# Kernel tuning notes

Hardware: AMD Instinct MI355X
Metric: run time of the kernel (lower is better)

Reference implementation:

```python
import jax, jax.numpy as jnp
import numpy as np

N = 50000
E = 800000
D = 128
EPS = 1e-5


def setup_inputs() -> dict:
    key = jax.random.key(0)
    ks = jax.random.split(key, 12)
    s1 = 1.0 / np.sqrt(2 * D)
    s2 = 1.0 / np.sqrt(D)
    return {
        "x": jax.random.normal(ks[0], (N, D), dtype=jnp.float32),
        "edge_index": jax.random.randint(ks[1], (2, E), 0, N, dtype=jnp.int32),
        # message MLP: Linear(2D->D), SiLU, Linear(D->D)
        "wm1": jax.random.uniform(ks[2], (2 * D, D), jnp.float32, -s1, s1),
        "bm1": jax.random.uniform(ks[3], (D,), jnp.float32, -s1, s1),
        "wm2": jax.random.uniform(ks[4], (D, D), jnp.float32, -s2, s2),
        "bm2": jax.random.uniform(ks[5], (D,), jnp.float32, -s2, s2),
        # update MLP: Linear(2D->D), SiLU, Linear(D->D)
        "wu1": jax.random.uniform(ks[6], (2 * D, D), jnp.float32, -s1, s1),
        "bu1": jax.random.uniform(ks[7], (D,), jnp.float32, -s1, s1),
        "wu2": jax.random.uniform(ks[8], (D, D), jnp.float32, -s2, s2),
        "bu2": jax.random.uniform(ks[9], (D,), jnp.float32, -s2, s2),
        # LayerNorm affine
        "gamma": jnp.ones((D,), jnp.float32),
        "beta": jnp.zeros((D,), jnp.float32),
    }


def reference(x, edge_index, wm1, bm1, wm2, bm2, wu1, bu1, wu2, bu2, gamma, beta):
    row, col = edge_index[0], edge_index[1]
    # gather endpoints and build message input [E, 2D]
    msg_in = jnp.concatenate([x[row], x[col]], axis=-1)
    h = jax.nn.silu(msg_in @ wm1 + bm1)
    messages = h @ wm2 + bm2  # [E, D]
    # scatter-add aggregate into destination rows
    aggr = jax.ops.segment_sum(messages, row, num_segments=x.shape[0])  # [N, D]
    upd_in = jnp.concatenate([x, aggr], axis=-1)  # [N, 2D]
    u = jax.nn.silu(upd_in @ wu1 + bu1)
    out = u @ wu2 + bu2  # [N, D]
    # residual + LayerNorm
    y = x + out
    mu = jnp.mean(y, axis=-1, keepdims=True)
    var = jnp.var(y, axis=-1, keepdims=True)
    yn = (y - mu) * jax.lax.rsqrt(var + EPS)
    return yn * gamma + beta
```

## Files before the change

### kernel.cpp

```cpp
#include <hip/hip_runtime.h>
#include <hip/hip_bf16.h>

#define NN 50000
#define EE 800000
#define DD 128
#define TILES (EE / 64)
#define NB_SCAN ((NN + 255) / 256)

typedef __attribute__((ext_vector_type(8))) short bf8v;
typedef __attribute__((ext_vector_type(4))) float f4v;
typedef __attribute__((ext_vector_type(4))) unsigned int u4v;

static __device__ __forceinline__ unsigned int bpack2(float lo, float hi) {
    union { __hip_bfloat162 h2; unsigned int u; } c;
    c.h2 = __float22bfloat162_rn(float2{lo, hi});
    return c.u;
}
static __device__ __forceinline__ u4v pack8(f4v a, f4v b) {
    u4v r;
    r[0] = bpack2(a[0], a[1]); r[1] = bpack2(a[2], a[3]);
    r[2] = bpack2(b[0], b[1]); r[3] = bpack2(b[2], b[3]);
    return r;
}
static __device__ __forceinline__ short f2bf_s(float f) {
    union { __hip_bfloat16 h; short s; } c;
    c.h = __float2bfloat16(f);
    return c.s;
}
static __device__ __forceinline__ float bf_lo(unsigned int u) {
    union { unsigned int u; float f; } c; c.u = u << 16; return c.f;
}
static __device__ __forceinline__ float bf_hi(unsigned int u) {
    union { unsigned int u; float f; } c; c.u = u & 0xffff0000u; return c.f;
}
static __device__ __forceinline__ float silu(float v) {
    return v * __builtin_amdgcn_rcpf(1.f + __expf(-v));
}

__global__ __launch_bounds__(256) void setup_kernel(
    const float* __restrict__ wm1, const float* __restrict__ wm2,
    const float* __restrict__ wu1, const float* __restrict__ wu2,
    short* __restrict__ out, int* __restrict__ cnt, float* __restrict__ aggr) {
    int idx = blockIdx.x * 256 + threadIdx.x;
    {
        const float* src; int l;
        if      (idx < 32768) { src = wm1; l = idx; }
        else if (idx < 49152) { src = wm2; l = idx - 32768; }
        else if (idx < 81920) { src = wu1; l = idx - 49152; }
        else                  { src = wu2; l = idx - 81920; }
        int e    = l & 7;
        int lane = (l >> 3) & 63;
        int ntg  = (l >> 9) & 7;
        int kc   = l >> 12;
        out[idx] = f2bf_s(src[(kc * 32 + (lane >> 4) * 8 + e) * DD + ntg * 16 + (lane & 15)]);
    }
    for (int i = idx; i < NN; i += 98304) cnt[i] = 0;
    f4v z = (f4v){0.f, 0.f, 0.f, 0.f};
    for (int i = idx; i < NN * DD / 4; i += 98304) ((f4v*)aggr)[i] = z;
}

__global__ __launch_bounds__(256) void hist_rank_kernel(const int* __restrict__ ei,
                                                        int* __restrict__ cnt,
                                                        int* __restrict__ rank) {
    int e = blockIdx.x * 256 + threadIdx.x;
    if (e < EE) rank[e] = atomicAdd(&cnt[ei[e]], 1);
}

__global__ __launch_bounds__(256) void scanA_kernel(const int* __restrict__ cnt,
                                                    int* __restrict__ bsum) {
    __shared__ int sd[256];
    int t = threadIdx.x;
    int i = blockIdx.x * 256 + t;
    sd[t] = (i < NN) ? cnt[i] : 0;
    __syncthreads();
    for (int off = 128; off > 0; off >>= 1) {
        if (t < off) sd[t] += sd[t + off];
        __syncthreads();
    }
    if (t == 0) bsum[blockIdx.x] = sd[0];
}

__global__ __launch_bounds__(256) void scanB_kernel(const int* __restrict__ bsum,
                                                    int* __restrict__ bscan) {
    __shared__ int sd[256];
    int t = threadIdx.x;
    int v = (t < NB_SCAN) ? bsum[t] : 0;
    sd[t] = v;
    __syncthreads();
    for (int off = 1; off < 256; off <<= 1) {
        int u = (t >= off) ? sd[t - off] : 0;
        __syncthreads();
        sd[t] += u;
        __syncthreads();
    }
    if (t < NB_SCAN) bscan[t] = sd[t] - v;
}

__global__ __launch_bounds__(256) void scanC_kernel(const int* __restrict__ cnt,
                                                    const int* __restrict__ bscan,
                                                    int* __restrict__ cursor,
                                                    int* __restrict__ rows) {
    __shared__ int sd[256];
    int t = threadIdx.x;
    int i = blockIdx.x * 256 + t;
    int v = (i < NN) ? cnt[i] : 0;
    sd[t] = v;
    __syncthreads();
    for (int off = 1; off < 256; off <<= 1) {
        int u = (t >= off) ? sd[t - off] : 0;
        __syncthreads();
        sd[t] += u;
        __syncthreads();
    }
    if (i < NN) {
        int c0 = bscan[blockIdx.x] + sd[t] - v;
        cursor[i] = c0;
        for (int k = 0; k < v; ++k) rows[c0 + k] = i;
    }
}

__global__ __launch_bounds__(256) void scatter_col_rank_kernel(const int* __restrict__ ei,
                                                               const int* __restrict__ cursor,
                                                               const int* __restrict__ rank,
                                                               int* __restrict__ srtc) {
    int e = blockIdx.x * 256 + threadIdx.x;
    if (e < EE) srtc[cursor[ei[e]] + rank[e]] = ei[EE + e];
}

__global__ __launch_bounds__(256) void scatter_col_atomic_kernel(const int* __restrict__ ei,
                                                                 int* __restrict__ cursor,
                                                                 int* __restrict__ srtc) {
    int e = blockIdx.x * 256 + threadIdx.x;
    if (e < EE) {
        int pos = atomicAdd(&cursor[ei[e]], 1);
        srtc[pos] = ei[EE + e];
    }
}

__global__ __launch_bounds__(256) void pq_kernel(
    const float* __restrict__ x,
    const short* __restrict__ W1f, const float* __restrict__ bm1,
    short* __restrict__ P, short* __restrict__ Q)
{
    __shared__ char smem[32768];
    const int tid = threadIdx.x;
    const int w = tid >> 6, lane = tid & 63;
    const int rbase = blockIdx.x * 64;
    const int rloc = tid >> 2, s = tid & 3;

    {
        int rg = rbase + rloc;
        int rgc = rg < NN ? rg : NN - 1;
        const float* xr = x + (size_t)rgc * DD + s * 32;
        int swz = (rloc & 7) << 4;
        #pragma unroll
        for (int j = 0; j < 4; ++j) {
            f4v a0 = *(const f4v*)(xr + j * 8);
            f4v a1 = *(const f4v*)(xr + j * 8 + 4);
            *(u4v*)(smem + ((rloc * 256 + s * 64 + j * 16) ^ swz)) = pack8(a0, a1);
        }
    }

    bf8v w1t[4][2], w1b[4][2];
    #pragma unroll
    for (int kc = 0; kc < 4; ++kc)
        #pragma unroll
        for (int nt = 0; nt < 2; ++nt) {
            w1t[kc][nt] = *(const bf8v*)(W1f + (((kc * 8) + (w * 2 + nt)) * 64 + lane) * 8);
            w1b[kc][nt] = *(const bf8v*)(W1f + ((((kc + 4) * 8) + (w * 2 + nt)) * 64 + lane) * 8);
        }
    __syncthreads();

    f4v accP[4][2], accQ[4][2];
    #pragma unroll
    for (int mt = 0; mt < 4; ++mt)
        #pragma unroll
        for (int nt = 0; nt < 2; ++nt) {
            accP[mt][nt] = (f4v){0.f, 0.f, 0.f, 0.f};
            accQ[mt][nt] = (f4v){0.f, 0.f, 0.f, 0.f};
        }
    #pragma unroll
    for (int kc = 0; kc < 4; ++kc) {
        bf8v a[4];
        int kb = kc * 64 + (lane >> 4) * 16;
        #pragma unroll
        for (int mt = 0; mt < 4; ++mt) {
            int row = mt * 16 + (lane & 15);
            a[mt] = *(const bf8v*)(smem + ((row * 256 + kb) ^ ((row & 7) << 4)));
        }
        #pragma unroll
        for (int mt = 0; mt < 4; ++mt)
            #pragma unroll
            for (int nt = 0; nt < 2; ++nt) {
                accP[mt][nt] = __builtin_amdgcn_mfma_f32_16x16x32_bf16(a[mt], w1t[kc][nt], accP[mt][nt], 0, 0, 0);
                accQ[mt][nt] = __builtin_amdgcn_mfma_f32_16x16x32_bf16(a[mt], w1b[kc][nt], accQ[mt][nt], 0, 0, 0);
            }
    }
    __syncthreads();

    int col0 = w * 32 + (lane & 15);
    float b1a = bm1[col0], b1b = bm1[col0 + 16];
    #pragma unroll
    for (int mt = 0; mt < 4; ++mt)
        #pragma unroll
        for (int nt = 0; nt < 2; ++nt) {
            float bb = nt ? b1b : b1a;
            int col = col0 + nt * 16;
            #pragma unroll
            for (int r = 0; r < 4; ++r) {
                int row = mt * 16 + (lane >> 4) * 4 + r;
                int off = (row * 256 + col * 2) ^ ((row & 7) << 4);
                *(short*)(smem + off)         = f2bf_s(accP[mt][nt][r] + bb);
                *(short*)(smem + 16384 + off) = f2bf_s(accQ[mt][nt][r]);
            }
        }
    __syncthreads();

    {
        int rg = rbase + rloc;
        if (rg < NN) {
            int swz = (rloc & 7) << 4;
            #pragma unroll
            for (int j = 0; j < 4; ++j) {
                int off = (rloc * 256 + s * 64 + j * 16) ^ swz;
                *(u4v*)(P + (size_t)rg * DD + s * 32 + j * 8) = *(const u4v*)(smem + off);
                *(u4v*)(Q + (size_t)rg * DD + s * 32 + j * 8) = *(const u4v*)(smem + 16384 + off);
            }
        }
    }
}

__global__ __launch_bounds__(256, 8) void edge_kernel(
    const short* __restrict__ P, const short* __restrict__ Q,
    const int* __restrict__ rows, const int* __restrict__ srtc,
    const int* __restrict__ ei, int use_sorted,
    const short* __restrict__ W2f, const float* __restrict__ bm2,
    float* __restrict__ aggr)
{
    __shared__ char smem[16384 + 256];
    char* Hs = smem;
    int* rows_s = (int*)(smem + 16384);

    const int tid = threadIdx.x;
    const int w = tid >> 6, lane = tid & 63;
    const int rloc = tid >> 2, s = tid & 3;

    {
        int eg = blockIdx.x * 64 + rloc;
        int r, c;
        if (use_sorted) { r = rows[eg]; c = srtc[eg]; }
        else            { r = ei[eg];   c = ei[EE + eg]; }
        if (s == 0) rows_s[rloc] = r;
        const u4v* pr = (const u4v*)(P + (size_t)r * DD + s * 32);
        const u4v* qr = (const u4v*)(Q + (size_t)c * DD + s * 32);
        int swz = (rloc & 7) << 4;
        #pragma unroll
        for (int j = 0; j < 4; ++j) {
            u4v pj = pr[j], qj = qr[j];
            u4v hv;
            #pragma unroll
            for (int k2 = 0; k2 < 4; ++k2) {
                float lo = silu(bf_lo(pj[k2]) + bf_lo(qj[k2]));
                float hi = silu(bf_hi(pj[k2]) + bf_hi(qj[k2]));
                hv[k2] = bpack2(lo, hi);
            }
            *(u4v*)(Hs + ((rloc * 256 + s * 64 + j * 16) ^ swz)) = hv;
        }
    }

    bf8v w2f[4][2];
    #pragma unroll
    for (int kc = 0; kc < 4; ++kc)
        #pragma unroll
        for (int nt = 0; nt < 2; ++nt)
            w2f[kc][nt] = *(const bf8v*)(W2f + (((kc * 8) + (w * 2 + nt)) * 64 + lane) * 8);
    int col0 = w * 32 + (lane & 15);
    float b2a = bm2[col0], b2b = bm2[col0 + 16];

    __syncthreads();

    f4v acc2[4][2];
    #pragma unroll
    for (int mt = 0; mt < 4; ++mt)
        #pragma unroll
        for (int nt = 0; nt < 2; ++nt)
            acc2[mt][nt] = (f4v){0.f, 0.f, 0.f, 0.f};
    #pragma unroll
    for (int kc = 0; kc < 4; ++kc) {
        bf8v a[4];
        int kb = kc * 64 + (lane >> 4) * 16;
        #pragma unroll
        for (int mt = 0; mt < 4; ++mt) {
            int row = mt * 16 + (lane & 15);
            a[mt] = *(const bf8v*)(Hs + ((row * 256 + kb) ^ ((row & 7) << 4)));
        }
        #pragma unroll
        for (int mt = 0; mt < 4; ++mt)
            #pragma unroll
            for (int nt = 0; nt < 2; ++nt)
                acc2[mt][nt] = __builtin_amdgcn_mfma_f32_16x16x32_bf16(a[mt], w2f[kc][nt], acc2[mt][nt], 0, 0, 0);
    }
    __syncthreads();

    #pragma unroll
    for (int mt = 0; mt < 4; ++mt)
        #pragma unroll
        for (int nt = 0; nt < 2; ++nt) {
            int col = col0 + nt * 16;
            float bb = nt ? b2b : b2a;
            #pragma unroll
            for (int r = 0; r < 4; ++r) {
                int row = mt * 16 + (lane >> 4) * 4 + r;
                *(short*)(Hs + ((row * 256 + col * 2) ^ ((row & 7) << 4))) = f2bf_s(acc2[mt][nt][r] + bb);
            }
        }
    __syncthreads();

    {
        int col = tid & 127;
        int r0 = (tid >> 7) * 32;
        int cur = rows_s[r0];
        float run = 0.f;
        for (int k = 0; k < 32; ++k) {
            int row = r0 + k;
            int d = rows_s[row];
            unsigned short sv = *(const unsigned short*)(Hs + ((row * 256 + col * 2) ^ ((row & 7) << 4)));
            union { unsigned int u; float f; } c; c.u = ((unsigned int)sv) << 16;
            if (d != cur) {
                unsafeAtomicAdd(aggr + (size_t)cur * DD + col, run);
                run = 0.f; cur = d;
            }
            run += c.f;
        }
        unsafeAtomicAdd(aggr + (size_t)cur * DD + col, run);
    }
}

__global__ __launch_bounds__(256, 4) void node_kernel(
    const float* __restrict__ x, const float* __restrict__ aggr,
    const short* __restrict__ U1f, const short* __restrict__ U2f,
    const float* __restrict__ bu1, const float* __restrict__ bu2,
    const float* __restrict__ gmm, const float* __restrict__ bta,
    float* __restrict__ out)
{
    __shared__ char smem[64 * 512 + 2048];
    char* As = smem;
    float* ps  = (float*)(smem + 64 * 512);
    float* ps2 = ps + 256;

    const int tid = threadIdx.x;
    const int w = tid >> 6, lane = tid & 63;
    const int rbase = blockIdx.x * 64;
    const int rloc = tid >> 2, s = tid & 3;

    {
        int rg = rbase + rloc;
        int rgc = rg < NN ? rg : 0;
        const float* xr = x + (size_t)rgc * DD + s * 32;
        const float* ar = aggr + (size_t)rgc * DD + s * 32;
        int swz = (rloc & 7) << 4;
        #pragma unroll
        for (int i2 = 0; i2 < 4; ++i2) {
            f4v a0 = *(const f4v*)(xr + i2 * 8);
            f4v a1 = *(const f4v*)(xr + i2 * 8 + 4);
            int addr = rloc * 512 + s * 64 + i2 * 16;
            *(u4v*)(As + (addr ^ swz)) = pack8(a0, a1);
            f4v b0 = *(const f4v*)(ar + i2 * 8);
            f4v b1 = *(const f4v*)(ar + i2 * 8 + 4);
            int addr2 = rloc * 512 + 256 + s * 64 + i2 * 16;
            *(u4v*)(As + (addr2 ^ swz)) = pack8(b0, b1);
        }
    }

    bf8v u1f[8][2], u2f[4][2];
    #pragma unroll
    for (int kc = 0; kc < 8; ++kc)
        #pragma unroll
        for (int nt = 0; nt < 2; ++nt)
            u1f[kc][nt] = *(const bf8v*)(U1f + (((kc * 8) + (w * 2 + nt)) * 64 + lane) * 8);
    #pragma unroll
    for (int kc = 0; kc < 4; ++kc)
        #pragma unroll
        for (int nt = 0; nt < 2; ++nt)
            u2f[kc][nt] = *(const bf8v*)(U2f + (((kc * 8) + (w * 2 + nt)) * 64 + lane) * 8);

    __syncthreads();

    f4v acc[4][2];
    #pragma unroll
    for (int mt = 0; mt < 4; ++mt)
        #pragma unroll
        for (int nt = 0; nt < 2; ++nt)
            acc[mt][nt] = (f4v){0.f, 0.f, 0.f, 0.f};
    #pragma unroll
    for (int kc = 0; kc < 8; ++kc) {
        bf8v a[4];
        int kb = kc * 64 + (lane >> 4) * 16;
        #pragma unroll
        for (int mt = 0; mt < 4; ++mt) {
            int row = mt * 16 + (lane & 15);
            a[mt] = *(const bf8v*)(As + ((row * 512 + kb) ^ ((row & 7) << 4)));
        }
        #pragma unroll
        for (int mt = 0; mt < 4; ++mt)
            #pragma unroll
            for (int nt = 0; nt < 2; ++nt)
                acc[mt][nt] = __builtin_amdgcn_mfma_f32_16x16x32_bf16(a[mt], u1f[kc][nt], acc[mt][nt], 0, 0, 0);
    }
    __syncthreads();

    int col0 = w * 32 + (lane & 15);
    float b1a = bu1[col0], b1b = bu1[col0 + 16];
    #pragma unroll
    for (int mt = 0; mt < 4; ++mt)
        #pragma unroll
        for (int nt = 0; nt < 2; ++nt) {
            float bb = nt ? b1b : b1a;
            int col = col0 + nt * 16;
            #pragma unroll
            for (int r = 0; r < 4; ++r) {
                float v = silu(acc[mt][nt][r] + bb);
                int row = mt * 16 + (lane >> 4) * 4 + r;
                *(short*)(As + ((row * 256 + col * 2) ^ ((row & 7) << 4))) = f2bf_s(v);
            }
        }
    __syncthreads();

    f4v acc2[4][2];
    #pragma unroll
    for (int mt = 0; mt < 4; ++mt)
        #pragma unroll
        for (int nt = 0; nt < 2; ++nt)
            acc2[mt][nt] = (f4v){0.f, 0.f, 0.f, 0.f};
    #pragma unroll
    for (int kc = 0; kc < 4; ++kc) {
        bf8v a[4];
        int kb = kc * 64 + (lane >> 4) * 16;
        #pragma unroll
        for (int mt = 0; mt < 4; ++mt) {
            int row = mt * 16 + (lane & 15);
            a[mt] = *(const bf8v*)(As + ((row * 256 + kb) ^ ((row & 7) << 4)));
        }
        #pragma unroll
        for (int mt = 0; mt < 4; ++mt)
            #pragma unroll
            for (int nt = 0; nt < 2; ++nt)
                acc2[mt][nt] = __builtin_amdgcn_mfma_f32_16x16x32_bf16(a[mt], u2f[kc][nt], acc2[mt][nt], 0, 0, 0);
    }
    __syncthreads();

    float b2a = bu2[col0], b2b = bu2[col0 + 16];
    #pragma unroll
    for (int mt = 0; mt < 4; ++mt)
        #pragma unroll
        for (int nt = 0; nt < 2; ++nt) {
            int col = col0 + nt * 16;
            float bb = nt ? b2b : b2a;
            #pragma unroll
            for (int r = 0; r < 4; ++r) {
                int rowl = mt * 16 + (lane >> 4) * 4 + r;
                int rg = rbase + rowl;
                int rgc = rg < NN ? rg : 0;
                float xv = x[(size_t)rgc * DD + col];
                float y = acc2[mt][nt][r] + bb + xv;
                *(float*)(As + ((rowl * 512 + col * 4) ^ ((rowl & 7) << 4))) = y;
            }
        }
    __syncthreads();

    {
        int q = tid & 3;
        float s1 = 0.f, s2 = 0.f;
        #pragma unroll
        for (int i = 0; i < 8; ++i) {
            f4v v = *(const f4v*)(As + ((rloc * 512 + q * 128 + i * 16) ^ ((rloc & 7) << 4)));
            s1 += v[0] + v[1] + v[2] + v[3];
            s2 += v[0] * v[0] + v[1] * v[1] + v[2] * v[2] + v[3] * v[3];
        }
        ps[rloc * 4 + q] = s1;
        ps2[rloc * 4 + q] = s2;
    }
    __syncthreads();
    {
        int q = tid & 3;
        float fs  = ps[rloc * 4] + ps[rloc * 4 + 1] + ps[rloc * 4 + 2] + ps[rloc * 4 + 3];
        float fs2 = ps2[rloc * 4] + ps2[rloc * 4 + 1] + ps2[rloc * 4 + 2] + ps2[rloc * 4 + 3];
        float mu  = fs * (1.f / 128.f);
        float var = fs2 * (1.f / 128.f) - mu * mu;
        float inv = rsqrtf(var + 1e-5f);
        int rg = rbase + rloc;
        if (rg < NN) {
            #pragma unroll
            for (int i = 0; i < 8; ++i) {
                int col = q * 32 + i * 4;
                f4v v  = *(const f4v*)(As + ((rloc * 512 + col * 4) ^ ((rloc & 7) << 4)));
                f4v gg = *(const f4v*)(gmm + col);
                f4v bb = *(const f4v*)(bta + col);
                f4v o;
                #pragma unroll
                for (int j = 0; j < 4; ++j)
                    o[j] = (v[j] - mu) * inv * gg[j] + bb[j];
                *(f4v*)(out + (size_t)rg * DD + col) = o;
            }
        }
    }
}

extern "C" void kernel_launch(void* const* d_in, const int* in_sizes, int n_in,
                              void* d_out, int out_size, void* d_ws, size_t ws_size,
                              hipStream_t stream) {
    const float* x    = (const float*)d_in[0];
    const int*   ei   = (const int*)d_in[1];
    const float* wm1  = (const float*)d_in[2];
    const float* bm1  = (const float*)d_in[3];
    const float* wm2  = (const float*)d_in[4];
    const float* bm2  = (const float*)d_in[5];
    const float* wu1  = (const float*)d_in[6];
    const float* bu1  = (const float*)d_in[7];
    const float* wu2  = (const float*)d_in[8];
    const float* bu2  = (const float*)d_in[9];
    const float* gmm  = (const float*)d_in[10];
    const float* bta  = (const float*)d_in[11];
    float* out = (float*)d_out;

    const size_t off_P     = 0;
    const size_t off_Q     = 12800000;
    const size_t off_frags = 25600000;
    const size_t off_cnt   = 25796608;
    const size_t off_cur   = 25996608;
    const size_t off_bsum  = 26196608;
    const size_t off_bscan = 26197632;
    const size_t off_rows  = 26198656;
    const size_t off_srtc  = 29398656;
    const size_t off_rank  = 32598656;
    const size_t need_rank   = 35798656;
    const size_t need_atomic = 32598656;

    char* wsB = (char*)d_ws;
    short* P    = (short*)(wsB + off_P);
    short* Q    = (short*)(wsB + off_Q);
    short* Wf   = (short*)(wsB + off_frags);
    short* W1f  = Wf;
    short* W2f  = Wf + 32768;
    short* U1f  = Wf + 49152;
    short* U2f  = Wf + 81920;
    int*   cnt    = (int*)(wsB + off_cnt);
    int*   cursor = (int*)(wsB + off_cur);
    int*   bsum   = (int*)(wsB + off_bsum);
    int*   bscan  = (int*)(wsB + off_bscan);
    int*   rows   = (int*)(wsB + off_rows);
    int*   srtc   = (int*)(wsB + off_srtc);
    int*   rank   = (int*)(wsB + off_rank);

    float* aggr = (float*)d_out;

    int tier = (ws_size >= need_rank) ? 2 : (ws_size >= need_atomic ? 1 : 0);

    setup_kernel<<<384, 256, 0, stream>>>(wm1, wm2, wu1, wu2, Wf, cnt, aggr);

    int use_sorted = 0;
    if (tier > 0) {
        hist_rank_kernel<<<(EE + 255) / 256, 256, 0, stream>>>(ei, cnt,
            tier == 2 ? rank : srtc );
        scanA_kernel<<<NB_SCAN, 256, 0, stream>>>(cnt, bsum);
        scanB_kernel<<<1, 256, 0, stream>>>(bsum, bscan);
        scanC_kernel<<<NB_SCAN, 256, 0, stream>>>(cnt, bscan, cursor, rows);
        if (tier == 2)
            scatter_col_rank_kernel<<<(EE + 255) / 256, 256, 0, stream>>>(ei, cursor, rank, srtc);
        else
            scatter_col_atomic_kernel<<<(EE + 255) / 256, 256, 0, stream>>>(ei, cursor, srtc);
        use_sorted = 1;
    }

    pq_kernel<<<(NN + 63) / 64, 256, 0, stream>>>(x, W1f, bm1, P, Q);

    edge_kernel<<<TILES, 256, 0, stream>>>(P, Q, rows, srtc, ei, use_sorted, W2f, bm2, aggr);
    node_kernel<<<(NN + 63) / 64, 256, 0, stream>>>(x, aggr, U1f, U2f, bu1, bu2, gmm, bta, out);
}
```

Measured before the change: 196.6 us.

## Merge preprocessing launches into fused kernels and shrink index arrays to 16-bit

Several kernels are merged so fewer launches run. The histogram/rank pass now shares a launch with weight fragment packing and aggr zeroing, and the column scatter shares a launch with the P/Q projection. The block-sum scan is folded into the second scan kernel, and cnt is cleared with a memset. Sorted row and column indices are stored as 16-bit values, halving index traffic in the edge kernel. The tier-1 atomic fallback is dropped. The u16 indices only hold because NN (50000) is below 65536.

```diff
diff --git a/kernel.cpp b/kernel.cpp
--- a/kernel.cpp
+++ b/kernel.cpp
@@ -6,6 +6,9 @@
 #define DD 128
 #define TILES (EE / 64)
 #define NB_SCAN ((NN + 255) / 256)
+#define HIST_BLKS ((EE + 255) / 256)
+#define FRAG_BLKS 384
+#define PQ_BLKS ((NN + 63) / 64)
 
 typedef __attribute__((ext_vector_type(8))) short bf8v;
 typedef __attribute__((ext_vector_type(4))) float f4v;
@@ -37,11 +40,21 @@
     return v * __builtin_amdgcn_rcpf(1.f + __expf(-v));
 }
 
-__global__ __launch_bounds__(256) void setup_kernel(
+__global__ __launch_bounds__(256) void mega1_kernel(
+    const int* __restrict__ ei, int* __restrict__ cnt, int* __restrict__ rank, int do_sort,
     const float* __restrict__ wm1, const float* __restrict__ wm2,
     const float* __restrict__ wu1, const float* __restrict__ wu2,
-    short* __restrict__ out, int* __restrict__ cnt, float* __restrict__ aggr) {
-    int idx = blockIdx.x * 256 + threadIdx.x;
+    short* __restrict__ wf, float* __restrict__ aggr)
+{
+    int b = blockIdx.x;
+    if (b < HIST_BLKS) {
+        if (do_sort) {
+            int e = b * 256 + threadIdx.x;
+            if (e < EE) rank[e] = atomicAdd(&cnt[ei[e]], 1);
+        }
+        return;
+    }
+    int idx = (b - HIST_BLKS) * 256 + threadIdx.x;
     {
         const float* src; int l;
         if      (idx < 32768) { src = wm1; l = idx; }
@@ -52,18 +65,10 @@
         int lane = (l >> 3) & 63;
         int ntg  = (l >> 9) & 7;
         int kc   = l >> 12;
-        out[idx] = f2bf_s(src[(kc * 32 + (lane >> 4) * 8 + e) * DD + ntg * 16 + (lane & 15)]);
-    }
-    for (int i = idx; i < NN; i += 98304) cnt[i] = 0;
+        wf[idx] = f2bf_s(src[(kc * 32 + (lane >> 4) * 8 + e) * DD + ntg * 16 + (lane & 15)]);
+    }
     f4v z = (f4v){0.f, 0.f, 0.f, 0.f};
-    for (int i = idx; i < NN * DD / 4; i += 98304) ((f4v*)aggr)[i] = z;
-}
-
-__global__ __launch_bounds__(256) void hist_rank_kernel(const int* __restrict__ ei,
-                                                        int* __restrict__ cnt,
-                                                        int* __restrict__ rank) {
-    int e = blockIdx.x * 256 + threadIdx.x;
-    if (e < EE) rank[e] = atomicAdd(&cnt[ei[e]], 1);
+    for (int i = idx; i < NN * DD / 4; i += FRAG_BLKS * 256) ((f4v*)aggr)[i] = z;
 }
 
 __global__ __launch_bounds__(256) void scanA_kernel(const int* __restrict__ cnt,
@@ -80,11 +85,25 @@
     if (t == 0) bsum[blockIdx.x] = sd[0];
 }
 
-__global__ __launch_bounds__(256) void scanB_kernel(const int* __restrict__ bsum,
-                                                    int* __restrict__ bscan) {
+__global__ __launch_bounds__(256) void scanC2_kernel(const int* __restrict__ cnt,
+                                                     const int* __restrict__ bsum,
+                                                     int* __restrict__ cursor,
+                                                     unsigned short* __restrict__ rows16) {
+    __shared__ int sb[256];
     __shared__ int sd[256];
     int t = threadIdx.x;
-    int v = (t < NB_SCAN) ? bsum[t] : 0;
+    sb[t] = (t < NB_SCAN) ? bsum[t] : 0;
+    __syncthreads();
+    for (int off = 1; off < 256; off <<= 1) {
+        int u = (t >= off) ? sb[t - off] : 0;
+        __syncthreads();
+        sb[t] += u;
+        __syncthreads();
+    }
+    int blockpre = (blockIdx.x == 0) ? 0 : sb[blockIdx.x - 1];
+    __syncthreads();
+    int i = blockIdx.x * 256 + t;
+    int v = (i < NN) ? cnt[i] : 0;
     sd[t] = v;
     __syncthreads();
     for (int off = 1; off < 256; off <<= 1) {
@@ -93,59 +112,31 @@
         sd[t] += u;
         __syncthreads();
     }
-    if (t < NB_SCAN) bscan[t] = sd[t] - v;
-}
-
-__global__ __launch_bounds__(256) void scanC_kernel(const int* __restrict__ cnt,
-                                                    const int* __restrict__ bscan,
-                                                    int* __restrict__ cursor,
-                                                    int* __restrict__ rows) {
-    __shared__ int sd[256];
-    int t = threadIdx.x;
-    int i = blockIdx.x * 256 + t;
-    int v = (i < NN) ? cnt[i] : 0;
-    sd[t] = v;
-    __syncthreads();
-    for (int off = 1; off < 256; off <<= 1) {
-        int u = (t >= off) ? sd[t - off] : 0;
-        __syncthreads();
-        sd[t] += u;
-        __syncthreads();
-    }
     if (i < NN) {
-        int c0 = bscan[blockIdx.x] + sd[t] - v;
+        int c0 = blockpre + sd[t] - v;
         cursor[i] = c0;
-        for (int k = 0; k < v; ++k) rows[c0 + k] = i;
-    }
-}
-
-__global__ __launch_bounds__(256) void scatter_col_rank_kernel(const int* __restrict__ ei,
-                                                               const int* __restrict__ cursor,
-                                                               const int* __restrict__ rank,
-                                                               int* __restrict__ srtc) {
-    int e = blockIdx.x * 256 + threadIdx.x;
-    if (e < EE) srtc[cursor[ei[e]] + rank[e]] = ei[EE + e];
-}
-
-__global__ __launch_bounds__(256) void scatter_col_atomic_kernel(const int* __restrict__ ei,
-                                                                 int* __restrict__ cursor,
-                                                                 int* __restrict__ srtc) {
-    int e = blockIdx.x * 256 + threadIdx.x;
-    if (e < EE) {
-        int pos = atomicAdd(&cursor[ei[e]], 1);
-        srtc[pos] = ei[EE + e];
-    }
-}
-
-__global__ __launch_bounds__(256) void pq_kernel(
-    const float* __restrict__ x,
-    const short* __restrict__ W1f, const float* __restrict__ bm1,
+        for (int k = 0; k < v; ++k) rows16[c0 + k] = (unsigned short)i;
+    }
+}
+
+__global__ __launch_bounds__(256) void mega2_kernel(
+    const int* __restrict__ ei, const int* __restrict__ cursor, const int* __restrict__ rank,
+    unsigned short* __restrict__ srtc16, int do_sort,
+    const float* __restrict__ x, const short* __restrict__ W1f, const float* __restrict__ bm1,
     short* __restrict__ P, short* __restrict__ Q)
 {
     __shared__ char smem[32768];
+    int b = blockIdx.x;
+    if (b < HIST_BLKS) {
+        if (do_sort) {
+            int e = b * 256 + threadIdx.x;
+            if (e < EE) srtc16[cursor[ei[e]] + rank[e]] = (unsigned short)ei[EE + e];
+        }
+        return;
+    }
     const int tid = threadIdx.x;
     const int w = tid >> 6, lane = tid & 63;
-    const int rbase = blockIdx.x * 64;
+    const int rbase = (b - HIST_BLKS) * 64;
     const int rloc = tid >> 2, s = tid & 3;
 
     {
@@ -232,7 +223,7 @@
 
 __global__ __launch_bounds__(256, 8) void edge_kernel(
     const short* __restrict__ P, const short* __restrict__ Q,
-    const int* __restrict__ rows, const int* __restrict__ srtc,
+    const unsigned short* __restrict__ rows16, const unsigned short* __restrict__ srtc16,
     const int* __restrict__ ei, int use_sorted,
     const short* __restrict__ W2f, const float* __restrict__ bm2,
     float* __restrict__ aggr)
@@ -248,8 +239,8 @@
     {
         int eg = blockIdx.x * 64 + rloc;
         int r, c;
-        if (use_sorted) { r = rows[eg]; c = srtc[eg]; }
-        else            { r = ei[eg];   c = ei[EE + eg]; }
+        if (use_sorted) { r = rows16[eg]; c = srtc16[eg]; }
+        else            { r = ei[eg];     c = ei[EE + eg]; }
         if (s == 0) rows_s[rloc] = r;
         const u4v* pr = (const u4v*)(P + (size_t)r * DD + s * 32);
         const u4v* qr = (const u4v*)(Q + (size_t)c * DD + s * 32);
@@ -523,18 +514,16 @@
     const float* bta  = (const float*)d_in[11];
     float* out = (float*)d_out;
 
-    const size_t off_P     = 0;
-    const size_t off_Q     = 12800000;
-    const size_t off_frags = 25600000;
-    const size_t off_cnt   = 25796608;
-    const size_t off_cur   = 25996608;
-    const size_t off_bsum  = 26196608;
-    const size_t off_bscan = 26197632;
-    const size_t off_rows  = 26198656;
-    const size_t off_srtc  = 29398656;
-    const size_t off_rank  = 32598656;
-    const size_t need_rank   = 35798656;
-    const size_t need_atomic = 32598656;
+    const size_t off_P      = 0;
+    const size_t off_Q      = 12800000;
+    const size_t off_frags  = 25600000;
+    const size_t off_cnt    = 25796608;
+    const size_t off_cur    = 25996608;
+    const size_t off_bsum   = 26196608;
+    const size_t off_rows16 = 26197632;
+    const size_t off_srtc16 = 27797632;
+    const size_t off_rank   = 29397632;
+    const size_t need_sort  = 32597632;
 
     char* wsB = (char*)d_ws;
     short* P    = (short*)(wsB + off_P);
@@ -547,33 +536,25 @@
     int*   cnt    = (int*)(wsB + off_cnt);
     int*   cursor = (int*)(wsB + off_cur);
     int*   bsum   = (int*)(wsB + off_bsum);
-    int*   bscan  = (int*)(wsB + off_bscan);
-    int*   rows   = (int*)(wsB + off_rows);
-    int*   srtc   = (int*)(wsB + off_srtc);
+    unsigned short* rows16 = (unsigned short*)(wsB + off_rows16);
+    unsigned short* srtc16 = (unsigned short*)(wsB + off_srtc16);
     int*   rank   = (int*)(wsB + off_rank);
 
     float* aggr = (float*)d_out;
 
-    int tier = (ws_size >= need_rank) ? 2 : (ws_size >= need_atomic ? 1 : 0);
-
-    setup_kernel<<<384, 256, 0, stream>>>(wm1, wm2, wu1, wu2, Wf, cnt, aggr);
-
-    int use_sorted = 0;
-    if (tier > 0) {
-        hist_rank_kernel<<<(EE + 255) / 256, 256, 0, stream>>>(ei, cnt,
-            tier == 2 ? rank : srtc );
+    int do_sort = (ws_size >= need_sort) ? 1 : 0;
+
+    hipMemsetAsync(cnt, 0, (size_t)NN * 4, stream);
+    mega1_kernel<<<HIST_BLKS + FRAG_BLKS, 256, 0, stream>>>(
+        ei, cnt, rank, do_sort, wm1, wm2, wu1, wu2, Wf, aggr);
+
+    if (do_sort) {
         scanA_kernel<<<NB_SCAN, 256, 0, stream>>>(cnt, bsum);
-        scanB_kernel<<<1, 256, 0, stream>>>(bsum, bscan);
-        scanC_kernel<<<NB_SCAN, 256, 0, stream>>>(cnt, bscan, cursor, rows);
-        if (tier == 2)
-            scatter_col_rank_kernel<<<(EE + 255) / 256, 256, 0, stream>>>(ei, cursor, rank, srtc);
-        else
-            scatter_col_atomic_kernel<<<(EE + 255) / 256, 256, 0, stream>>>(ei, cursor, srtc);
-        use_sorted = 1;
-    }
-
-    pq_kernel<<<(NN + 63) / 64, 256, 0, stream>>>(x, W1f, bm1, P, Q);
-
-    edge_kernel<<<TILES, 256, 0, stream>>>(P, Q, rows, srtc, ei, use_sorted, W2f, bm2, aggr);
+        scanC2_kernel<<<NB_SCAN, 256, 0, stream>>>(cnt, bsum, cursor, rows16);
+    }
+    mega2_kernel<<<HIST_BLKS + PQ_BLKS, 256, 0, stream>>>(
+        ei, cursor, rank, srtc16, do_sort, x, W1f, bm1, P, Q);
+
+    edge_kernel<<<TILES, 256, 0, stream>>>(P, Q, rows16, srtc16, ei, do_sort, W2f, bm2, aggr);
     node_kernel<<<(NN + 63) / 64, 256, 0, stream>>>(x, aggr, U1f, U2f, bu1, bu2, gmm, bta, out);
 }
```

Result: faster. 191.9 us, median of 2 (-2.4%).
